# Optimization experiments

Measured on AMD Instinct MI355X. Metric: run time of the kernel, lower is better.

Reference implementation:

```python
import jax, jax.numpy as jnp
import numpy as np

B, S, HID = 1, 2048, 2304
H, KV, D = 8, 4, 256
FF = 9216
CAP = 50.0                      # attn_logit_softcapping
SCALE = 256.0 ** -0.5           # query_pre_attn_scalar ** -0.5
WIN = 1024                      # sliding_window_size
EPS = 1e-6
NEG = -2.3819763e38


def setup_inputs() -> dict:
    key = jax.random.key(0)
    ks = jax.random.split(key, 11)
    w = lambda k, shp: jax.random.normal(k, shp, jnp.float32) * 0.02
    ln = lambda k: jax.random.normal(k, (HID,), jnp.float32) * 0.1
    hidden_states = jax.random.normal(ks[0], (B, S, HID), jnp.float32)
    qkv_w = w(ks[1], (HID, (H + 2 * KV) * D))
    o_w = w(ks[2], (H * D, HID))
    gate_w = w(ks[3], (HID, FF))
    up_w = w(ks[4], (HID, FF))
    down_w = w(ks[5], (FF, HID))
    in_ln_w = ln(ks[6]); post_attn_ln_w = ln(ks[7])
    pre_ffw_ln_w = ln(ks[8]); post_ffw_ln_w = ln(ks[9])
    # precompute_freqs_cis (theta=10000) as cos/sin of shape [S, D//2]
    inv = 1.0 / (10000.0 ** (np.arange(0, D, 2)[: D // 2].astype(np.float64) / D))
    fr = np.outer(np.arange(S), inv)
    cos = jnp.asarray(np.cos(fr), jnp.float32)
    sin = jnp.asarray(np.sin(fr), jnp.float32)
    kv_write_indices = jnp.arange(S, dtype=jnp.int32)
    k_cache = jnp.zeros((B, S, KV, D), jnp.float32)
    v_cache = jnp.zeros((B, S, KV, D), jnp.float32)
    causal = jnp.tril(jnp.ones((S, S), bool))
    mask = jnp.where(causal, 0.0, NEG).astype(jnp.float32)[None, None]
    return dict(hidden_states=hidden_states, qkv_w=qkv_w, o_w=o_w,
                gate_w=gate_w, up_w=up_w, down_w=down_w,
                in_ln_w=in_ln_w, post_attn_ln_w=post_attn_ln_w,
                pre_ffw_ln_w=pre_ffw_ln_w, post_ffw_ln_w=post_ffw_ln_w,
                cos=cos, sin=sin, kv_write_indices=kv_write_indices,
                k_cache=k_cache, v_cache=v_cache, mask=mask)


def rmsnorm(x, wt):
    x = x.astype(jnp.float32)
    x = x * jax.lax.rsqrt(jnp.mean(x * x, axis=-1, keepdims=True) + EPS)
    return x * (1.0 + wt)  # add_unit_offset=True


def rope(x, cos, sin):
    # x: [b,s,h,d]; complex rotation with real=first half, imag=second half
    x1, x2 = jnp.split(x, 2, axis=-1)
    c = cos[None, :, None, :]
    s = sin[None, :, None, :]
    return jnp.concatenate([x1 * c - x2 * s, x1 * s + x2 * c], axis=-1)


def reference(hidden_states, qkv_w, o_w, gate_w, up_w, down_w,
              in_ln_w, post_attn_ln_w, pre_ffw_ln_w, post_ffw_ln_w,
              cos, sin, kv_write_indices, k_cache, v_cache, mask):
    residual = hidden_states
    x = rmsnorm(hidden_states, in_ln_w)
    qkv = x @ qkv_w
    q = qkv[..., : H * D].reshape(B, S, H, D)
    k = qkv[..., H * D: H * D + KV * D].reshape(B, S, KV, D)
    v = qkv[..., H * D + KV * D:].reshape(B, S, KV, D)
    q = rope(q, cos, sin)
    k = rope(k, cos, sin)
    kc = k_cache.at[:, kv_write_indices].set(k)
    vc = v_cache.at[:, kv_write_indices].set(v)
    g = H // KV
    kr = jnp.repeat(kc, g, axis=2)   # GQA repeat_interleave -> [B,S,H,D]
    vr = jnp.repeat(vc, g, axis=2)
    scores = jnp.einsum('bqhd,bkhd->bhqk', q * SCALE, kr)
    pos = jnp.arange(S)
    band = jnp.abs(pos[:, None] - pos[None, :]) <= (WIN - 1)
    m = jnp.where(band[None, None], mask, NEG)
    scores = jnp.tanh(scores / CAP) * CAP + m
    probs = jax.nn.softmax(scores.astype(jnp.float32), axis=-1)
    attn = jnp.einsum('bhqk,bkhd->bqhd', probs, vr).reshape(B, S, H * D)
    attn = attn @ o_w
    h = residual + rmsnorm(attn, post_attn_ln_w)
    residual = h
    x = rmsnorm(h, pre_ffw_ln_w)
    x = jax.nn.gelu(x @ gate_w, approximate=True) * (x @ up_w)
    x = x @ down_w
    x = rmsnorm(x, post_ffw_ln_w)
    return residual + x
```

## Files before the change

### kernel.cpp

```cpp
#include <hip/hip_runtime.h>
#include <hip/hip_bf16.h>
#include <cstdint>
#include <cstddef>

#define S_LEN  2048
#define HIDDEN 2304
#define NHEAD  8
#define NKVH   4
#define DHEAD  256
#define FFDIM  9216
#define QKVN   4096
#define ODIM   2048
#define WINM1  1023
#define QSCALE 0.0625f
#define CAPF   50.0f
#define PSTR   ((size_t)S_LEN * HIDDEN)

typedef __attribute__((ext_vector_type(4))) float f32x4;
typedef __attribute__((ext_vector_type(8))) short s16x8;

__device__ __forceinline__ void gload_lds16(const void* gptr, void* lptr) {
  __builtin_amdgcn_global_load_lds(
      (const __attribute__((address_space(1))) unsigned int*)gptr,
      (__attribute__((address_space(3))) unsigned int*)lptr, 16, 0, 0);
}

__global__ void k_fill(float* p, float v, size_t n) {
  size_t i = (size_t)blockIdx.x * blockDim.x + threadIdx.x;
  size_t st = (size_t)gridDim.x * blockDim.x;
  for (; i < n; i += st) p[i] = v;
}

__global__ void k_transpose_bf16(const float* __restrict__ in, __hip_bfloat16* __restrict__ out,
                                 int R, int C) {
  __shared__ float tile[32][33];
  const int c0 = blockIdx.x * 32, r0 = blockIdx.y * 32;
  const int tc = threadIdx.x & 31, tr = threadIdx.x >> 5;
#pragma unroll
  for (int i = 0; i < 4; i++)
    tile[tr + 8 * i][tc] = in[(size_t)(r0 + tr + 8 * i) * C + c0 + tc];
  __syncthreads();
#pragma unroll
  for (int i = 0; i < 4; i++)
    out[(size_t)(c0 + tr + 8 * i) * R + r0 + tc] = __float2bfloat16(tile[tc][tr + 8 * i]);
}

template <int NP, bool INBF16, bool ADD, bool BF16OUT>
__global__ void k_rmsnorm(const void* __restrict__ xv, const float* __restrict__ w,
                          const float* __restrict__ res, void* __restrict__ outv) {
  const int row = blockIdx.x;
  __shared__ float xs[HIDDEN];
  float ss = 0.f;
  for (int i = threadIdx.x; i < HIDDEN; i += 256) {
    float v = 0.f;
#pragma unroll
    for (int p = 0; p < NP; p++) {
      if constexpr (INBF16)
        v += __bfloat162float(((const __hip_bfloat16*)xv)[(size_t)p * PSTR + (size_t)row * HIDDEN + i]);
      else
        v += ((const float*)xv)[(size_t)p * PSTR + (size_t)row * HIDDEN + i];
    }
    xs[i] = v;
    ss += v * v;
  }
#pragma unroll
  for (int off = 32; off >= 1; off >>= 1) ss += __shfl_down(ss, off);
  __shared__ float red[4];
  __shared__ float srstd;
  if ((threadIdx.x & 63) == 0) red[threadIdx.x >> 6] = ss;
  __syncthreads();
  if (threadIdx.x == 0) {
    float tot = red[0] + red[1] + red[2] + red[3];
    srstd = rsqrtf(tot / (float)HIDDEN + 1e-6f);
  }
  __syncthreads();
  const float rstd = srstd;
  for (int i = threadIdx.x; i < HIDDEN; i += 256) {
    float v = xs[i] * rstd * (1.f + w[i]);
    if constexpr (ADD) v += res[(size_t)row * HIDDEN + i];
    if constexpr (BF16OUT)
      ((__hip_bfloat16*)outv)[(size_t)row * HIDDEN + i] = __float2bfloat16(v);
    else
      ((float*)outv)[(size_t)row * HIDDEN + i] = v;
  }
}

template <int EPI>
__global__ __launch_bounds__(256) void k_gemm_bt(const __hip_bfloat16* __restrict__ A,
                                                 const __hip_bfloat16* __restrict__ Bt,
                                                 void* __restrict__ Cv,
                                                 const __hip_bfloat16* __restrict__ G,
                                                 int N, int K) {
  __shared__ alignas(16) __hip_bfloat16 sA[128 * 64];
  __shared__ alignas(16) __hip_bfloat16 sB[128 * 64];
  const int t = threadIdx.x;
  const int w = t >> 6;
  const int wm = w >> 1, wn = w & 1;
  const int nwg = gridDim.x * gridDim.y;
  const int fblk = blockIdx.y * gridDim.x + blockIdx.x;
  const int qq = nwg >> 3, r8 = nwg & 7;
  const int xcd = fblk & 7, ix = fblk >> 3;
  const int swz = (xcd < r8 ? xcd * (qq + 1) : r8 * (qq + 1) + (xcd - r8) * qq) + ix;
  const int m0 = (swz % gridDim.y) * 128, n0 = (swz / gridDim.y) * 128;
  const int lr = t & 15, lg = (t & 63) >> 4;
  const int srow = t >> 3, sc8 = t & 7;

  f32x4 acc[4][4];
#pragma unroll
  for (int a = 0; a < 4; a++)
#pragma unroll
    for (int b = 0; b < 4; b++) acc[a][b] = (f32x4){0.f, 0.f, 0.f, 0.f};

  for (int kt = 0; kt < K; kt += 64) {
#pragma unroll
    for (int i = 0; i < 4; i++) {
      const __hip_bfloat16* g = A + (size_t)(m0 + i * 32 + srow) * K + kt + sc8 * 8;
      gload_lds16(g, sA + (size_t)(i * 256 + w * 64) * 8);
    }
#pragma unroll
    for (int i = 0; i < 4; i++) {
      const __hip_bfloat16* g = Bt + (size_t)(n0 + i * 32 + srow) * K + kt + sc8 * 8;
      gload_lds16(g, sB + (size_t)(i * 256 + w * 64) * 8);
    }
    __syncthreads();
#pragma unroll
    for (int ks = 0; ks < 2; ks++) {
      s16x8 af[4], bfr[4];
#pragma unroll
      for (int fm = 0; fm < 4; fm++)
        af[fm] = *reinterpret_cast<const s16x8*>(sA + (wm * 64 + fm * 16 + lr) * 64 + ks * 32 + lg * 8);
#pragma unroll
      for (int fn = 0; fn < 4; fn++)
        bfr[fn] = *reinterpret_cast<const s16x8*>(sB + (wn * 64 + fn * 16 + lr) * 64 + ks * 32 + lg * 8);
#pragma unroll
      for (int fm = 0; fm < 4; fm++)
#pragma unroll
        for (int fn = 0; fn < 4; fn++)
          acc[fm][fn] = __builtin_amdgcn_mfma_f32_16x16x32_bf16(af[fm], bfr[fn], acc[fm][fn], 0, 0, 0);
    }
    __syncthreads();
  }
#pragma unroll
  for (int fm = 0; fm < 4; fm++) {
    const int rb = m0 + wm * 64 + fm * 16 + lg * 4;
#pragma unroll
    for (int fn = 0; fn < 4; fn++) {
      const int col = n0 + wn * 64 + fn * 16 + lr;
#pragma unroll
      for (int j = 0; j < 4; j++) {
        const size_t idx = (size_t)(rb + j) * N + col;
        if constexpr (EPI == 0) {
          ((float*)Cv)[idx] = acc[fm][fn][j];
        } else if constexpr (EPI == 1) {
          ((__hip_bfloat16*)Cv)[idx] = __float2bfloat16(acc[fm][fn][j]);
        } else {
          const float x = __bfloat162float(G[idx]);
          const float tt = tanhf(0.7978845608028654f * (x + 0.044715f * x * x * x));
          ((__hip_bfloat16*)Cv)[idx] = __float2bfloat16(0.5f * x * (1.f + tt) * acc[fm][fn][j]);
        }
      }
    }
  }
}

template <int EPI>
__global__ __launch_bounds__(512, 2) void k_gemm8(const __hip_bfloat16* __restrict__ A,
                                                  const __hip_bfloat16* __restrict__ Bt,
                                                  void* __restrict__ Cv,
                                                  const __hip_bfloat16* __restrict__ G,
                                                  const __hip_bfloat16* __restrict__ Bt2,
                                                  void* __restrict__ Cv2,
                                                  int N, int K, int keff) {
  __shared__ alignas(16) __hip_bfloat16 smem[65536];
  const int t = threadIdx.x;
  const int w = t >> 6;
  const int wm = w >> 2, wn = w & 3;
  const int l = t & 63;
  const int lr = l & 15, lg = l >> 4;

  const int nxy = gridDim.x * gridDim.y;
  const int nwg = nxy * gridDim.z;
  const int fblk = blockIdx.z * nxy + blockIdx.y * gridDim.x + blockIdx.x;
  const int qq = nwg >> 3, r8 = nwg & 7;
  const int xcd = fblk & 7, ix = fblk >> 3;
  const int swz = (xcd < r8 ? xcd * (qq + 1) : r8 * (qq + 1) + (xcd - r8) * qq) + ix;
  const int plane = swz / nxy;
  const int rem = swz % nxy;
  const int m0 = (rem % gridDim.y) * 256, n0 = (rem / gridDim.y) * 256;
  const int k0 = plane * keff;

  const __hip_bfloat16* Bsrc = Bt;
  int nb0 = n0;
  if constexpr (EPI == 3) {
    if (n0 >= FFDIM) { Bsrc = Bt2; nb0 = n0 - FFDIM; }
  }

  const int sA8 = l & 7;
  size_t aoff[2], boff[2];
#pragma unroll
  for (int j = 0; j < 2; j++) {
    const int rv = (w * 2 + j) * 8 + (l >> 3);
    const int ko = (sA8 ^ (rv & 7)) * 8;
    aoff[j] = (size_t)(m0 + ((rv >> 6) & 1) * 128 + ((rv >> 4) & 3) * 16 + (rv & 15)) * K + k0 + ko;
    boff[j] = (size_t)(nb0 + ((rv >> 5) & 3) * 64 + ((rv >> 4) & 1) * 16 + (rv & 15)) * K + k0 + ko;
  }
  const int sl0 = ((lg) ^ (lr & 7)) * 8;
  const int sl1 = ((4 + lg) ^ (lr & 7)) * 8;

  f32x4 acc[8][4];
#pragma unroll
  for (int a = 0; a < 8; a++)
#pragma unroll
    for (int b = 0; b < 4; b++) acc[a][b] = (f32x4){0.f, 0.f, 0.f, 0.f};
  s16x8 af[4][2], bf[2][2];

#define STG_A(bu, h, kti) { _Pragma("unroll") for (int j = 0; j < 2; j++) \
    gload_lds16(A + aoff[j] + (size_t)(h) * 64 * K + (size_t)(kti) * 64, \
                smem + (bu) * 32768 + (h) * 8192 + (w * 2 + j) * 512); }
#define STG_B(bu, h, kti) { _Pragma("unroll") for (int j = 0; j < 2; j++) \
    gload_lds16(Bsrc + boff[j] + (size_t)(h) * 32 * K + (size_t)(kti) * 64, \
                smem + (bu) * 32768 + 16384 + (h) * 8192 + (w * 2 + j) * 512); }
#define RD_A(bu, fmh) { const __hip_bfloat16* ab_ = smem + (bu) * 32768; \
    _Pragma("unroll") for (int f2 = 0; f2 < 4; f2++) { \
      const int ro_ = ((fmh) * 128 + wm * 64 + f2 * 16 + lr) * 64; \
      af[f2][0] = *(const s16x8*)(ab_ + ro_ + sl0); \
      af[f2][1] = *(const s16x8*)(ab_ + ro_ + sl1); } }
#define RD_B(bu, fnh) { const __hip_bfloat16* bb_ = smem + (bu) * 32768 + 16384; \
    _Pragma("unroll") for (int f2 = 0; f2 < 2; f2++) { \
      const int ro_ = ((fnh) * 128 + wn * 32 + f2 * 16 + lr) * 64; \
      bf[f2][0] = *(const s16x8*)(bb_ + ro_ + sl0); \
      bf[f2][1] = *(const s16x8*)(bb_ + ro_ + sl1); } }
#define MFMA16(fmh, fnh) { __builtin_amdgcn_s_setprio(1); \
    _Pragma("unroll") for (int f2 = 0; f2 < 4; f2++) \
    _Pragma("unroll") for (int g2 = 0; g2 < 2; g2++) \
    _Pragma("unroll") for (int ks = 0; ks < 2; ks++) \
      acc[(fmh) * 4 + f2][(fnh) * 2 + g2] = __builtin_amdgcn_mfma_f32_16x16x32_bf16( \
          af[f2][ks], bf[g2][ks], acc[(fmh) * 4 + f2][(fnh) * 2 + g2], 0, 0, 0); \
    __builtin_amdgcn_s_setprio(0); }
#define BARR() asm volatile("s_barrier" ::: "memory")
#define LGKM0() asm volatile("s_waitcnt lgkmcnt(0)" ::: "memory")
#define VMC4() asm volatile("s_waitcnt vmcnt(4)" ::: "memory")
#define VMC0() asm volatile("s_waitcnt vmcnt(0)" ::: "memory")

  STG_A(0, 0, 0); STG_A(0, 1, 0); STG_B(0, 0, 0); STG_B(0, 1, 0);
  STG_A(1, 0, 1); STG_A(1, 1, 1);
  VMC4(); BARR();

  const int niter = keff >> 7;
  for (int i = 0; i < niter; ++i) {
    const int t1 = 2 * i + 1;
    const bool more = (i + 1 < niter);
    RD_A(0, 0); RD_B(0, 0);
    STG_B(1, 0, t1);
    BARR(); LGKM0(); MFMA16(0, 0); BARR();
    RD_B(0, 1);
    STG_B(1, 1, t1);
    if (more) STG_A(0, 0, t1 + 1);
    BARR(); LGKM0(); MFMA16(0, 1); BARR();
    RD_A(0, 1); RD_B(0, 0);
    BARR(); LGKM0(); MFMA16(1, 0); BARR();
    RD_B(0, 1);
    if (more) STG_A(0, 1, t1 + 1);
    BARR(); LGKM0(); MFMA16(1, 1);
    if (more) { VMC4(); } else { VMC0(); }
    BARR();
    RD_A(1, 0); RD_B(1, 0);
    if (more) STG_B(0, 0, t1 + 1);
    BARR(); LGKM0(); MFMA16(0, 0); BARR();
    RD_B(1, 1);
    if (more) STG_B(0, 1, t1 + 1);
    BARR(); LGKM0(); MFMA16(0, 1); BARR();
    RD_A(1, 1); RD_B(1, 0);
    if (more) STG_A(1, 0, t1 + 2);
    BARR(); LGKM0(); MFMA16(1, 0); BARR();
    RD_B(1, 1);
    if (more) STG_A(1, 1, t1 + 2);
    BARR(); LGKM0(); MFMA16(1, 1);
    if (more) { VMC4(); }
    BARR();
  }
#undef STG_A
#undef STG_B
#undef RD_A
#undef RD_B
#undef MFMA16
#undef BARR
#undef LGKM0
#undef VMC4
#undef VMC0

  __hip_bfloat16* Cw = nullptr;
  int cbase = n0, cstride = N;
  if constexpr (EPI == 3) {
    Cw = (__hip_bfloat16*)((n0 < FFDIM) ? Cv : Cv2);
    cbase = (n0 < FFDIM) ? n0 : n0 - FFDIM;
    cstride = FFDIM;
  }
#pragma unroll
  for (int fm = 0; fm < 8; fm++) {
    const int rb = m0 + wm * 128 + fm * 16 + lg * 4;
#pragma unroll
    for (int fn = 0; fn < 4; fn++) {
      const int coln = wn * 64 + fn * 16 + lr;
#pragma unroll
      for (int j = 0; j < 4; j++) {
        if constexpr (EPI == 3) {
          Cw[(size_t)(rb + j) * cstride + cbase + coln] = __float2bfloat16(acc[fm][fn][j]);
        } else {
          const size_t idxo = (size_t)(rb + j) * N + n0 + coln;
          if constexpr (EPI == 0) {
            ((float*)Cv)[idxo] = acc[fm][fn][j];
          } else if constexpr (EPI == 1) {
            ((__hip_bfloat16*)Cv)[idxo] = __float2bfloat16(acc[fm][fn][j]);
          } else if constexpr (EPI == 2) {
            const float x = __bfloat162float(G[idxo]);
            const float tg = tanhf(0.7978845608028654f * (x + 0.044715f * x * x * x));
            ((__hip_bfloat16*)Cv)[idxo] = __float2bfloat16(0.5f * x * (1.f + tg) * acc[fm][fn][j]);
          } else if constexpr (EPI == 4) {
            float* P = (plane == 0) ? (float*)Cv : (float*)Cv2;
            P[idxo] = acc[fm][fn][j];
          } else {
            ((__hip_bfloat16*)Cv)[(size_t)plane * PSTR + idxo] = __float2bfloat16(acc[fm][fn][j]);
          }
        }
      }
    }
  }
}

__global__ void k_gelu_mul2(const __hip_bfloat16* __restrict__ g, const __hip_bfloat16* __restrict__ u,
                            __hip_bfloat16* __restrict__ o, int n8) {
  const int st = gridDim.x * blockDim.x;
  for (int i = blockIdx.x * blockDim.x + threadIdx.x; i < n8; i += st) {
    s16x8 gv = *(const s16x8*)(g + (size_t)i * 8);
    s16x8 uv = *(const s16x8*)(u + (size_t)i * 8);
    s16x8 ov;
#pragma unroll
    for (int j = 0; j < 8; j++) {
      const float x = __uint_as_float(((uint32_t)(uint16_t)gv[j]) << 16);
      const float uu = __uint_as_float(((uint32_t)(uint16_t)uv[j]) << 16);
      const float tt = tanhf(0.7978845608028654f * (x + 0.044715f * x * x * x));
      const float r = 0.5f * x * (1.f + tt) * uu;
      ov[j] = (short)(__hip_bfloat16_raw(__float2bfloat16(r)).x);
    }
    *(s16x8*)(o + (size_t)i * 8) = ov;
  }
}

__global__ void k_rope_split(const float* __restrict__ p0, const float* __restrict__ p1,
                             const float* __restrict__ cosb, const float* __restrict__ sinb,
                             __hip_bfloat16* __restrict__ qo, __hip_bfloat16* __restrict__ ko) {
  const int s = blockIdx.x;
  const float* r0 = p0 + (size_t)s * QKVN;
  const float* r1 = p1 + (size_t)s * QKVN;
  const float* cr = cosb + (size_t)s * 128;
  const float* sr = sinb + (size_t)s * 128;
  for (int idx = threadIdx.x; idx < (NHEAD + NKVH) * 128; idx += 256) {
    const int hh = idx >> 7, d = idx & 127;
    const float cv = cr[d], sv = sr[d];
    if (hh < NHEAD) {
      const float x1 = r0[hh * DHEAD + d] + r1[hh * DHEAD + d];
      const float x2 = r0[hh * DHEAD + 128 + d] + r1[hh * DHEAD + 128 + d];
      const size_t base = ((size_t)hh * S_LEN + s) * DHEAD;
      qo[base + d]       = __float2bfloat16((x1 * cv - x2 * sv) * QSCALE);
      qo[base + 128 + d] = __float2bfloat16((x1 * sv + x2 * cv) * QSCALE);
    } else {
      const int kv = hh - NHEAD;
      const int o1 = NHEAD * DHEAD + kv * DHEAD + d;
      const float x1 = r0[o1] + r1[o1];
      const float x2 = r0[o1 + 128] + r1[o1 + 128];
      const size_t base = ((size_t)kv * S_LEN + s) * DHEAD;
      ko[base + d]       = __float2bfloat16(x1 * cv - x2 * sv);
      ko[base + 128 + d] = __float2bfloat16(x1 * sv + x2 * cv);
    }
  }
}

__global__ __launch_bounds__(256) void k_vsplit_t(const float* __restrict__ p0,
                                                  const float* __restrict__ p1,
                                                  __hip_bfloat16* __restrict__ vt) {
  __shared__ float tile[64][260];
  const int s0 = blockIdx.x * 64, kv = blockIdx.y;
  const int t = threadIdx.x;
  const int rr = t >> 6, c4 = t & 63;
#pragma unroll
  for (int p = 0; p < 16; p++) {
    const int row = rr + p * 4;
    const size_t go = (size_t)(s0 + row) * QKVN + (NHEAD + NKVH) * DHEAD + kv * DHEAD + c4 * 4;
    const float4 v0 = *(const float4*)(p0 + go);
    const float4 v1 = *(const float4*)(p1 + go);
    float4 v;
    v.x = v0.x + v1.x; v.y = v0.y + v1.y; v.z = v0.z + v1.z; v.w = v0.w + v1.w;
    *(float4*)(&tile[row][c4 * 4]) = v;
  }
  __syncthreads();
  const int c = t & 31, dr = t >> 5;
#pragma unroll
  for (int p = 0; p < 32; p++) {
    const int d = dr + p * 8;
    __hip_bfloat162 pr;
    pr.x = __float2bfloat16(tile[2 * c][d]);
    pr.y = __float2bfloat16(tile[2 * c + 1][d]);
    *(__hip_bfloat162*)(vt + ((size_t)kv * DHEAD + d) * S_LEN + s0 + 2 * c) = pr;
  }
}

__global__ __launch_bounds__(256) void k_attn_mfma(const __hip_bfloat16* __restrict__ Q,
                                                   const __hip_bfloat16* __restrict__ Kb,
                                                   const __hip_bfloat16* __restrict__ Vt,
                                                   __hip_bfloat16* __restrict__ O) {
  __shared__ alignas(16) __hip_bfloat16 Ks[64 * 264];
  __shared__ alignas(16) __hip_bfloat16 Vs[256 * 72];
  __shared__ alignas(16) __hip_bfloat16 Ps[64 * 72];
  const int h = blockIdx.y, kvh = h >> 1;
  const int q0 = blockIdx.x * 64;
  const int t = threadIdx.x;
  const int wq = t >> 6;
  const int l = t & 63;
  const int lr = l & 15, lg = l >> 4;

  s16x8 qf[8];
  {
    const __hip_bfloat16* qrow = Q + ((size_t)h * S_LEN + q0 + wq * 16 + lr) * DHEAD;
#pragma unroll
    for (int ks = 0; ks < 8; ks++) qf[ks] = *(const s16x8*)(qrow + ks * 32 + lg * 8);
  }
  f32x4 acc[16];
#pragma unroll
  for (int i = 0; i < 16; i++) acc[i] = (f32x4){0.f, 0.f, 0.f, 0.f};
  float rsum[4] = {0.f, 0.f, 0.f, 0.f};

  int lo = q0 - WINM1;
  if (lo < 0) lo = 0;
  lo &= ~63;
  const int qrow_base = q0 + wq * 16 + lg * 4;

  for (int kc = lo; kc <= q0; kc += 64) {
#pragma unroll
    for (int p = 0; p < 8; p++) {
      const int idx = t + p * 256;
      const int row = idx >> 5, c16 = idx & 31;
      s16x8 v = *(const s16x8*)(Kb + ((size_t)kvh * S_LEN + kc + row) * DHEAD + c16 * 8);
      *(s16x8*)(Ks + row * 264 + c16 * 8) = v;
    }
#pragma unroll
    for (int p = 0; p < 8; p++) {
      const int idx = t + p * 256;
      const int d = idx >> 3, ch = idx & 7;
      s16x8 v = *(const s16x8*)(Vt + ((size_t)kvh * DHEAD + d) * S_LEN + kc + ch * 8);
      *(s16x8*)(Vs + d * 72 + ch * 8) = v;
    }
    __syncthreads();

    f32x4 sc[4];
#pragma unroll
    for (int fq = 0; fq < 4; fq++) {
      sc[fq] = (f32x4){0.f, 0.f, 0.f, 0.f};
#pragma unroll
      for (int ks = 0; ks < 8; ks++) {
        s16x8 bfr = *(const s16x8*)(Ks + (fq * 16 + lr) * 264 + ks * 32 + lg * 8);
        sc[fq] = __builtin_amdgcn_mfma_f32_16x16x32_bf16(qf[ks], bfr, sc[fq], 0, 0, 0);
      }
    }
#pragma unroll
    for (int fq = 0; fq < 4; fq++) {
      const int k = kc + fq * 16 + lr;
#pragma unroll
      for (int j = 0; j < 4; j++) {
        const int qw = qrow_base + j;
        float p = 0.f;
        if (k <= qw && qw - k <= WINM1) {
          const float s = sc[fq][j];
          const float u = exp2f(s * 0.057707801635558534f);
          const float arg = 72.134752044448169f -
                            144.26950408889634f * __builtin_amdgcn_rcpf(u + 1.f);
          p = exp2f(arg);
        }
        const __hip_bfloat16 pb = __float2bfloat16(p);
        Ps[(wq * 16 + lg * 4 + j) * 72 + fq * 16 + lr] = pb;
        rsum[j] += __bfloat162float(pb);
      }
    }
#pragma unroll
    for (int ks2 = 0; ks2 < 2; ks2++) {
      s16x8 pa = *(const s16x8*)(Ps + (wq * 16 + lr) * 72 + ks2 * 32 + lg * 8);
#pragma unroll
      for (int f2 = 0; f2 < 16; f2++) {
        s16x8 vb = *(const s16x8*)(Vs + (f2 * 16 + lr) * 72 + ks2 * 32 + lg * 8);
        acc[f2] = __builtin_amdgcn_mfma_f32_16x16x32_bf16(pa, vb, acc[f2], 0, 0, 0);
      }
    }
    __syncthreads();
  }
#pragma unroll
  for (int j = 0; j < 4; j++) {
    float s = rsum[j];
#pragma unroll
    for (int off = 1; off < 16; off <<= 1) s += __shfl_xor(s, off, 64);
    rsum[j] = 1.f / s;
  }
#pragma unroll
  for (int f2 = 0; f2 < 16; f2++)
#pragma unroll
    for (int j = 0; j < 4; j++)
      O[(size_t)(qrow_base + j) * ODIM + h * DHEAD + f2 * 16 + lr] =
          __float2bfloat16(acc[f2][j] * rsum[j]);
}

extern "C" void kernel_launch(void* const* d_in, const int* in_sizes, int n_in,
                              void* d_out, int out_size, void* d_ws, size_t ws_size,
                              hipStream_t stream) {
  const float* hidden  = (const float*)d_in[0];
  const float* qkv_w   = (const float*)d_in[1];
  const float* o_w     = (const float*)d_in[2];
  const float* gate_w  = (const float*)d_in[3];
  const float* up_w    = (const float*)d_in[4];
  const float* down_w  = (const float*)d_in[5];
  const float* in_ln   = (const float*)d_in[6];
  const float* post_attn_ln = (const float*)d_in[7];
  const float* pre_ffw_ln   = (const float*)d_in[8];
  const float* post_ffw_ln  = (const float*)d_in[9];
  const float* cosb    = (const float*)d_in[10];
  const float* sinb    = (const float*)d_in[11];
  float* out = (float*)d_out;
  char* ws = (char*)d_ws;

  const size_t OFF_W   = 0;
  const size_t OFF_HF  = 42467328;
  const size_t OFF_X   = 61341696;
  const size_t OFF_S1  = 70778880;
  const size_t OFF_S2  = 108527616;
  const size_t NEED    = 146276352;
  const size_t OFF_W2  = 146276352;
  const size_t NEED_F  = 188743680;

  if (ws_size < NEED) {
    k_fill<<<1024, 256, 0, stream>>>(out, 100000.0f + (float)(ws_size >> 20), (size_t)out_size);
    return;
  }
  const bool FUSED = (ws_size >= NEED_F);

  __hip_bfloat16* W    = (__hip_bfloat16*)(ws + OFF_W);
  __hip_bfloat16* W2   = (__hip_bfloat16*)(ws + OFF_W2);
  float*          Hf   = (float*)(ws + OFF_HF);
  __hip_bfloat16* Xb   = (__hip_bfloat16*)(ws + OFF_X);
  __hip_bfloat16* GATEB= (__hip_bfloat16*)(ws + OFF_S1);
  __hip_bfloat16* UPB  = (__hip_bfloat16*)(ws + OFF_S2);
  __hip_bfloat16* Qb   = (__hip_bfloat16*)(ws + OFF_S2);
  __hip_bfloat16* Kb   = (__hip_bfloat16*)(ws + OFF_S2 + 8388608);
  __hip_bfloat16* Vtb  = (__hip_bfloat16*)(ws + OFF_S2 + 12582912);
  __hip_bfloat16* ATTN = (__hip_bfloat16*)(ws + OFF_S2 + 29360128);

  if (FUSED) {
    float* QKV0 = (float*)(ws + OFF_S1);
    float* QKV1 = (float*)(ws + OFF_W2);
    float* PROJ = (float*)(ws + OFF_S1);
    __hip_bfloat16* DPART = (__hip_bfloat16*)(ws + OFF_S2);

    k_transpose_bf16<<<dim3(QKVN / 32, HIDDEN / 32), 256, 0, stream>>>(qkv_w, W, HIDDEN, QKVN);
    k_rmsnorm<1, false, false, true><<<S_LEN, 256, 0, stream>>>(hidden, in_ln, nullptr, Xb);
    k_gemm8<4><<<dim3(QKVN / 256, S_LEN / 256, 2), 512, 0, stream>>>(
        Xb, W, QKV0, nullptr, nullptr, QKV1, QKVN, HIDDEN, HIDDEN / 2);
    k_rope_split<<<S_LEN, 256, 0, stream>>>(QKV0, QKV1, cosb, sinb, Qb, Kb);
    k_vsplit_t<<<dim3(S_LEN / 64, NKVH), 256, 0, stream>>>(QKV0, QKV1, Vtb);
    k_attn_mfma<<<dim3(S_LEN / 64, NHEAD), 256, 0, stream>>>(Qb, Kb, Vtb, ATTN);
    k_transpose_bf16<<<dim3(HIDDEN / 32, ODIM / 32), 256, 0, stream>>>(o_w, W, ODIM, HIDDEN);
    k_gemm8<4><<<dim3(HIDDEN / 256, S_LEN / 256, 2), 512, 0, stream>>>(
        ATTN, W, PROJ, nullptr, nullptr, PROJ + PSTR, HIDDEN, ODIM, ODIM / 2);
    k_rmsnorm<2, false, true, false><<<S_LEN, 256, 0, stream>>>(PROJ, post_attn_ln, hidden, Hf);
    k_rmsnorm<1, false, false, true><<<S_LEN, 256, 0, stream>>>(Hf, pre_ffw_ln, nullptr, Xb);
    k_transpose_bf16<<<dim3(FFDIM / 32, HIDDEN / 32), 256, 0, stream>>>(gate_w, W, HIDDEN, FFDIM);
    k_transpose_bf16<<<dim3(FFDIM / 32, HIDDEN / 32), 256, 0, stream>>>(up_w, W2, HIDDEN, FFDIM);
    k_gemm8<3><<<dim3((2 * FFDIM) / 256, S_LEN / 256, 1), 512, 0, stream>>>(
        Xb, W, GATEB, nullptr, W2, UPB, FFDIM, HIDDEN, HIDDEN);
    k_gelu_mul2<<<2048, 256, 0, stream>>>(GATEB, UPB, GATEB, (S_LEN * FFDIM) / 8);
    k_transpose_bf16<<<dim3(HIDDEN / 32, FFDIM / 32), 256, 0, stream>>>(down_w, W, FFDIM, HIDDEN);
    k_gemm8<5><<<dim3(HIDDEN / 256, S_LEN / 256, 8), 512, 0, stream>>>(
        GATEB, W, DPART, nullptr, nullptr, nullptr, HIDDEN, FFDIM, FFDIM / 8);
    k_rmsnorm<8, true, true, false><<<S_LEN, 256, 0, stream>>>(DPART, post_ffw_ln, Hf, out);
  } else {
    float* QKV = (float*)(ws + OFF_S1);
    float* PROJ = (float*)(ws + OFF_S2);
    k_transpose_bf16<<<dim3(QKVN / 32, HIDDEN / 32), 256, 0, stream>>>(qkv_w, W, HIDDEN, QKVN);
    k_rmsnorm<1, false, false, true><<<S_LEN, 256, 0, stream>>>(hidden, in_ln, nullptr, Xb);
    k_gemm_bt<0><<<dim3(QKVN / 128, S_LEN / 128), 256, 0, stream>>>(Xb, W, QKV, nullptr, QKVN, HIDDEN);
    k_rope_split<<<S_LEN, 256, 0, stream>>>(QKV, QKV, cosb, sinb, Qb, Kb);
    k_fill<<<1024, 256, 0, stream>>>(Hf, 0.f, PSTR);
    k_rope_split<<<S_LEN, 256, 0, stream>>>(QKV, Hf, cosb, sinb, Qb, Kb);
    k_vsplit_t<<<dim3(S_LEN / 64, NKVH), 256, 0, stream>>>(QKV, Hf, Vtb);
    k_attn_mfma<<<dim3(S_LEN / 64, NHEAD), 256, 0, stream>>>(Qb, Kb, Vtb, ATTN);
    k_transpose_bf16<<<dim3(HIDDEN / 32, ODIM / 32), 256, 0, stream>>>(o_w, W, ODIM, HIDDEN);
    k_gemm_bt<0><<<dim3(HIDDEN / 128, S_LEN / 128), 256, 0, stream>>>(ATTN, W, PROJ, nullptr, HIDDEN, ODIM);
    k_rmsnorm<1, false, true, false><<<S_LEN, 256, 0, stream>>>(PROJ, post_attn_ln, hidden, Hf);
    k_rmsnorm<1, false, false, true><<<S_LEN, 256, 0, stream>>>(Hf, pre_ffw_ln, nullptr, Xb);
    k_transpose_bf16<<<dim3(FFDIM / 32, HIDDEN / 32), 256, 0, stream>>>(gate_w, W, HIDDEN, FFDIM);
    k_gemm8<1><<<dim3(FFDIM / 256, S_LEN / 256, 1), 512, 0, stream>>>(
        Xb, W, GATEB, nullptr, nullptr, nullptr, FFDIM, HIDDEN, HIDDEN);
    __hip_bfloat16* ACT = (__hip_bfloat16*)(ws + OFF_S2);
    k_transpose_bf16<<<dim3(FFDIM / 32, HIDDEN / 32), 256, 0, stream>>>(up_w, W, HIDDEN, FFDIM);
    k_gemm8<2><<<dim3(FFDIM / 256, S_LEN / 256, 1), 512, 0, stream>>>(
        Xb, W, ACT, GATEB, nullptr, nullptr, FFDIM, HIDDEN, HIDDEN);
    float* Yf = (float*)(ws + OFF_S1);
    k_transpose_bf16<<<dim3(HIDDEN / 32, FFDIM / 32), 256, 0, stream>>>(down_w, W, FFDIM, HIDDEN);
    k_gemm_bt<0><<<dim3(HIDDEN / 128, S_LEN / 128), 256, 0, stream>>>(ACT, W, Yf, nullptr, HIDDEN, FFDIM);
    k_rmsnorm<1, false, true, false><<<S_LEN, 256, 0, stream>>>(Yf, post_ffw_ln, Hf, out);
  }
}
```

Before: 700.2 us.

## Add half-height 128x256 GEMM kernel for FFN and fuse double rmsnorm

Adds k_gemm8h, a 128x256-tile variant of the 8-wave GEMM with a smaller LDS footprint and launch_bounds(512,2), so two workgroups can share a CU. It is used for the fused gate/up GEMM and the split-K down projection, which also doubles the number of tiles. The post-attention rmsnorm and pre-FFN rmsnorm are merged into one kernel to cut a launch and a round trip of the hidden state. The fallback path is trimmed and moved onto k_gemm_bt. The tradeoff is less data reuse per tile and extra A-tile loads.

```diff
diff --git a/kernel.cpp b/kernel.cpp
--- a/kernel.cpp
+++ b/kernel.cpp
@@ -83,6 +83,48 @@
     else
       ((float*)outv)[(size_t)row * HIDDEN + i] = v;
   }
+}
+
+__global__ void k_rmsnorm2(const float* __restrict__ planes, const float* __restrict__ w1,
+                           const float* __restrict__ res, const float* __restrict__ w2,
+                           float* __restrict__ hf, __hip_bfloat16* __restrict__ xb) {
+  const int row = blockIdx.x;
+  __shared__ float xs[HIDDEN];
+  __shared__ float red[4];
+  __shared__ float srstd;
+  float ss = 0.f;
+  for (int i = threadIdx.x; i < HIDDEN; i += 256) {
+    const float v = planes[(size_t)row * HIDDEN + i] + planes[PSTR + (size_t)row * HIDDEN + i];
+    xs[i] = v;
+    ss += v * v;
+  }
+#pragma unroll
+  for (int off = 32; off >= 1; off >>= 1) ss += __shfl_down(ss, off);
+  if ((threadIdx.x & 63) == 0) red[threadIdx.x >> 6] = ss;
+  __syncthreads();
+  if (threadIdx.x == 0)
+    srstd = rsqrtf((red[0] + red[1] + red[2] + red[3]) / (float)HIDDEN + 1e-6f);
+  __syncthreads();
+  const float rstd1 = srstd;
+  float ss2 = 0.f;
+  for (int i = threadIdx.x; i < HIDDEN; i += 256) {
+    const float h = res[(size_t)row * HIDDEN + i] + xs[i] * rstd1 * (1.f + w1[i]);
+    hf[(size_t)row * HIDDEN + i] = h;
+    ss2 += h * h;
+  }
+  __syncthreads();
+  for (int i = threadIdx.x; i < HIDDEN; i += 256)
+    xs[i] = hf[(size_t)row * HIDDEN + i];
+#pragma unroll
+  for (int off = 32; off >= 1; off >>= 1) ss2 += __shfl_down(ss2, off);
+  if ((threadIdx.x & 63) == 0) red[threadIdx.x >> 6] = ss2;
+  __syncthreads();
+  if (threadIdx.x == 0)
+    srstd = rsqrtf((red[0] + red[1] + red[2] + red[3]) / (float)HIDDEN + 1e-6f);
+  __syncthreads();
+  const float rstd2 = srstd;
+  for (int i = threadIdx.x; i < HIDDEN; i += 256)
+    xb[(size_t)row * HIDDEN + i] = __float2bfloat16(xs[i] * rstd2 * (1.f + w2[i]));
 }
 
 template <int EPI>
@@ -189,12 +231,6 @@
   const int m0 = (rem % gridDim.y) * 256, n0 = (rem / gridDim.y) * 256;
   const int k0 = plane * keff;
 
-  const __hip_bfloat16* Bsrc = Bt;
-  int nb0 = n0;
-  if constexpr (EPI == 3) {
-    if (n0 >= FFDIM) { Bsrc = Bt2; nb0 = n0 - FFDIM; }
-  }
-
   const int sA8 = l & 7;
   size_t aoff[2], boff[2];
 #pragma unroll
@@ -202,7 +238,7 @@
     const int rv = (w * 2 + j) * 8 + (l >> 3);
     const int ko = (sA8 ^ (rv & 7)) * 8;
     aoff[j] = (size_t)(m0 + ((rv >> 6) & 1) * 128 + ((rv >> 4) & 3) * 16 + (rv & 15)) * K + k0 + ko;
-    boff[j] = (size_t)(nb0 + ((rv >> 5) & 3) * 64 + ((rv >> 4) & 1) * 16 + (rv & 15)) * K + k0 + ko;
+    boff[j] = (size_t)(n0 + ((rv >> 5) & 3) * 64 + ((rv >> 4) & 1) * 16 + (rv & 15)) * K + k0 + ko;
   }
   const int sl0 = ((lg) ^ (lr & 7)) * 8;
   const int sl1 = ((4 + lg) ^ (lr & 7)) * 8;
@@ -218,7 +254,7 @@
     gload_lds16(A + aoff[j] + (size_t)(h) * 64 * K + (size_t)(kti) * 64, \
                 smem + (bu) * 32768 + (h) * 8192 + (w * 2 + j) * 512); }
 #define STG_B(bu, h, kti) { _Pragma("unroll") for (int j = 0; j < 2; j++) \
-    gload_lds16(Bsrc + boff[j] + (size_t)(h) * 32 * K + (size_t)(kti) * 64, \
+    gload_lds16(Bt + boff[j] + (size_t)(h) * 32 * K + (size_t)(kti) * 64, \
                 smem + (bu) * 32768 + 16384 + (h) * 8192 + (w * 2 + j) * 512); }
 #define RD_A(bu, fmh) { const __hip_bfloat16* ab_ = smem + (bu) * 32768; \
     _Pragma("unroll") for (int f2 = 0; f2 < 4; f2++) { \
@@ -289,41 +325,158 @@
 #undef VMC4
 #undef VMC0
 
-  __hip_bfloat16* Cw = nullptr;
-  int cbase = n0, cstride = N;
+#pragma unroll
+  for (int fm = 0; fm < 8; fm++) {
+    const int rb = m0 + wm * 128 + fm * 16 + lg * 4;
+#pragma unroll
+    for (int fn = 0; fn < 4; fn++) {
+      const int coln = wn * 64 + fn * 16 + lr;
+#pragma unroll
+      for (int j = 0; j < 4; j++) {
+        const size_t idxo = (size_t)(rb + j) * N + n0 + coln;
+        if constexpr (EPI == 4) {
+          float* P = (plane == 0) ? (float*)Cv : (float*)Cv2;
+          P[idxo] = acc[fm][fn][j];
+        } else {
+          ((__hip_bfloat16*)Cv)[idxo] = __float2bfloat16(acc[fm][fn][j]);
+        }
+      }
+    }
+  }
+}
+
+template <int EPI>
+__global__ __launch_bounds__(512, 2) void k_gemm8h(const __hip_bfloat16* __restrict__ A,
+                                                   const __hip_bfloat16* __restrict__ Bt,
+                                                   void* __restrict__ Cv,
+                                                   const __hip_bfloat16* __restrict__ Bt2,
+                                                   void* __restrict__ Cv2,
+                                                   int N, int K, int keff) {
+  __shared__ alignas(16) __hip_bfloat16 smem[49152];
+  const int t = threadIdx.x;
+  const int w = t >> 6;
+  const int wm = w >> 2, wn = w & 3;
+  const int l = t & 63;
+  const int lr = l & 15, lg = l >> 4;
+
+  const int nxy = gridDim.x * gridDim.y;
+  const int nwg = nxy * gridDim.z;
+  const int fblk = blockIdx.z * nxy + blockIdx.y * gridDim.x + blockIdx.x;
+  const int qq = nwg >> 3, r8 = nwg & 7;
+  const int xcd = fblk & 7, ix = fblk >> 3;
+  const int swz = (xcd < r8 ? xcd * (qq + 1) : r8 * (qq + 1) + (xcd - r8) * qq) + ix;
+  const int plane = swz / nxy;
+  const int rem = swz % nxy;
+  const int m0 = (rem % gridDim.y) * 128, n0 = (rem / gridDim.y) * 256;
+  const int k0 = plane * keff;
+
+  const __hip_bfloat16* Bsrc = Bt;
+  int nb0 = n0;
+  if constexpr (EPI == 3) {
+    if (n0 >= FFDIM) { Bsrc = Bt2; nb0 = n0 - FFDIM; }
+  }
+
+  const int lrow = w * 8 + (l >> 3);
+  const int ko = (((l & 7) ^ (l >> 3))) * 8;
+  const size_t aoffh = (size_t)(m0 + lrow) * K + k0 + ko;
+  const size_t boffh = (size_t)(nb0 + lrow) * K + k0 + ko;
+  const int sl0 = ((lg) ^ (lr & 7)) * 8;
+  const int sl1 = ((4 + lg) ^ (lr & 7)) * 8;
+
+  f32x4 acc[4][4];
+#pragma unroll
+  for (int a = 0; a < 4; a++)
+#pragma unroll
+    for (int b = 0; b < 4; b++) acc[a][b] = (f32x4){0.f, 0.f, 0.f, 0.f};
+  s16x8 af[4][2], bf[2][2];
+
+#define HSTG_A(bu, kti) { _Pragma("unroll") for (int j = 0; j < 2; j++) \
+    gload_lds16(A + aoffh + (size_t)j * 64 * K + (size_t)(kti) * 64, \
+                smem + (bu) * 24576 + (j * 64 + w * 8) * 64); }
+#define HSTG_B0(bu, kti) { _Pragma("unroll") for (int j = 0; j < 2; j++) \
+    gload_lds16(Bsrc + boffh + (size_t)j * 64 * K + (size_t)(kti) * 64, \
+                smem + (bu) * 24576 + 8192 + (j * 64 + w * 8) * 64); }
+#define HSTG_B1(bu, kti) { _Pragma("unroll") for (int j = 2; j < 4; j++) \
+    gload_lds16(Bsrc + boffh + (size_t)j * 64 * K + (size_t)(kti) * 64, \
+                smem + (bu) * 24576 + 8192 + (j * 64 + w * 8) * 64); }
+#define HRD_A(bu) { const __hip_bfloat16* ab_ = smem + (bu) * 24576; \
+    _Pragma("unroll") for (int f2 = 0; f2 < 4; f2++) { \
+      const int ro_ = (wm * 64 + f2 * 16 + lr) * 64; \
+      af[f2][0] = *(const s16x8*)(ab_ + ro_ + sl0); \
+      af[f2][1] = *(const s16x8*)(ab_ + ro_ + sl1); } }
+#define HRD_B(bu, fnh) { const __hip_bfloat16* bb_ = smem + (bu) * 24576 + 8192; \
+    _Pragma("unroll") for (int f2 = 0; f2 < 2; f2++) { \
+      const int ro_ = ((fnh) * 128 + wn * 32 + f2 * 16 + lr) * 64; \
+      bf[f2][0] = *(const s16x8*)(bb_ + ro_ + sl0); \
+      bf[f2][1] = *(const s16x8*)(bb_ + ro_ + sl1); } }
+#define HMFMA16(fnh) { __builtin_amdgcn_s_setprio(1); \
+    _Pragma("unroll") for (int f2 = 0; f2 < 4; f2++) \
+    _Pragma("unroll") for (int g2 = 0; g2 < 2; g2++) \
+    _Pragma("unroll") for (int ks = 0; ks < 2; ks++) \
+      acc[f2][(fnh) * 2 + g2] = __builtin_amdgcn_mfma_f32_16x16x32_bf16( \
+          af[f2][ks], bf[g2][ks], acc[f2][(fnh) * 2 + g2], 0, 0, 0); \
+    __builtin_amdgcn_s_setprio(0); }
+#define HBARR() asm volatile("s_barrier" ::: "memory")
+#define HLGKM0() asm volatile("s_waitcnt lgkmcnt(0)" ::: "memory")
+#define HVMC4() asm volatile("s_waitcnt vmcnt(4)" ::: "memory")
+#define HVMC0() asm volatile("s_waitcnt vmcnt(0)" ::: "memory")
+
+  HSTG_A(0, 0); HSTG_B0(0, 0); HSTG_B1(0, 0);
+  HSTG_A(1, 1); HSTG_B0(1, 1);
+  HVMC4(); HBARR();
+
+  const int niter = keff >> 7;
+  for (int i = 0; i < niter; ++i) {
+    const int t1 = 2 * i + 1;
+    const bool more = (i + 1 < niter);
+    HRD_A(0); HRD_B(0, 0);
+    HSTG_B1(1, t1);
+    HBARR(); HLGKM0(); HMFMA16(0); HBARR();
+    HRD_B(0, 1);
+    if (more) { HSTG_A(0, t1 + 1); HSTG_B0(0, t1 + 1); }
+    HBARR(); HLGKM0(); HMFMA16(1);
+    if (more) { HVMC4(); } else { HVMC0(); }
+    HBARR();
+    HRD_A(1); HRD_B(1, 0);
+    if (more) HSTG_B1(0, t1 + 1);
+    HBARR(); HLGKM0(); HMFMA16(0); HBARR();
+    HRD_B(1, 1);
+    if (more) { HSTG_A(1, t1 + 2); HSTG_B0(1, t1 + 2); }
+    HBARR(); HLGKM0(); HMFMA16(1);
+    if (more) { HVMC4(); }
+    HBARR();
+  }
+#undef HSTG_A
+#undef HSTG_B0
+#undef HSTG_B1
+#undef HRD_A
+#undef HRD_B
+#undef HMFMA16
+#undef HBARR
+#undef HLGKM0
+#undef HVMC4
+#undef HVMC0
+
+  __hip_bfloat16* Cw;
+  int cbase, cstride;
   if constexpr (EPI == 3) {
     Cw = (__hip_bfloat16*)((n0 < FFDIM) ? Cv : Cv2);
     cbase = (n0 < FFDIM) ? n0 : n0 - FFDIM;
     cstride = FFDIM;
-  }
-#pragma unroll
-  for (int fm = 0; fm < 8; fm++) {
-    const int rb = m0 + wm * 128 + fm * 16 + lg * 4;
+  } else {
+    Cw = (__hip_bfloat16*)Cv + (size_t)plane * PSTR;
+    cbase = n0;
+    cstride = N;
+  }
+#pragma unroll
+  for (int fm = 0; fm < 4; fm++) {
+    const int rb = m0 + wm * 64 + fm * 16 + lg * 4;
 #pragma unroll
     for (int fn = 0; fn < 4; fn++) {
-      const int coln = wn * 64 + fn * 16 + lr;
-#pragma unroll
-      for (int j = 0; j < 4; j++) {
-        if constexpr (EPI == 3) {
-          Cw[(size_t)(rb + j) * cstride + cbase + coln] = __float2bfloat16(acc[fm][fn][j]);
-        } else {
-          const size_t idxo = (size_t)(rb + j) * N + n0 + coln;
-          if constexpr (EPI == 0) {
-            ((float*)Cv)[idxo] = acc[fm][fn][j];
-          } else if constexpr (EPI == 1) {
-            ((__hip_bfloat16*)Cv)[idxo] = __float2bfloat16(acc[fm][fn][j]);
-          } else if constexpr (EPI == 2) {
-            const float x = __bfloat162float(G[idxo]);
-            const float tg = tanhf(0.7978845608028654f * (x + 0.044715f * x * x * x));
-            ((__hip_bfloat16*)Cv)[idxo] = __float2bfloat16(0.5f * x * (1.f + tg) * acc[fm][fn][j]);
-          } else if constexpr (EPI == 4) {
-            float* P = (plane == 0) ? (float*)Cv : (float*)Cv2;
-            P[idxo] = acc[fm][fn][j];
-          } else {
-            ((__hip_bfloat16*)Cv)[(size_t)plane * PSTR + idxo] = __float2bfloat16(acc[fm][fn][j]);
-          }
-        }
-      }
+      const int coln = (fn >> 1) * 128 + wn * 32 + (fn & 1) * 16 + lr;
+#pragma unroll
+      for (int j = 0; j < 4; j++)
+        Cw[(size_t)(rb + j) * cstride + cbase + coln] = __float2bfloat16(acc[fm][fn][j]);
     }
   }
 }
@@ -567,16 +720,15 @@
     k_transpose_bf16<<<dim3(HIDDEN / 32, ODIM / 32), 256, 0, stream>>>(o_w, W, ODIM, HIDDEN);
     k_gemm8<4><<<dim3(HIDDEN / 256, S_LEN / 256, 2), 512, 0, stream>>>(
         ATTN, W, PROJ, nullptr, nullptr, PROJ + PSTR, HIDDEN, ODIM, ODIM / 2);
-    k_rmsnorm<2, false, true, false><<<S_LEN, 256, 0, stream>>>(PROJ, post_attn_ln, hidden, Hf);
-    k_rmsnorm<1, false, false, true><<<S_LEN, 256, 0, stream>>>(Hf, pre_ffw_ln, nullptr, Xb);
+    k_rmsnorm2<<<S_LEN, 256, 0, stream>>>(PROJ, post_attn_ln, hidden, pre_ffw_ln, Hf, Xb);
     k_transpose_bf16<<<dim3(FFDIM / 32, HIDDEN / 32), 256, 0, stream>>>(gate_w, W, HIDDEN, FFDIM);
     k_transpose_bf16<<<dim3(FFDIM / 32, HIDDEN / 32), 256, 0, stream>>>(up_w, W2, HIDDEN, FFDIM);
-    k_gemm8<3><<<dim3((2 * FFDIM) / 256, S_LEN / 256, 1), 512, 0, stream>>>(
-        Xb, W, GATEB, nullptr, W2, UPB, FFDIM, HIDDEN, HIDDEN);
+    k_gemm8h<3><<<dim3((2 * FFDIM) / 256, S_LEN / 128, 1), 512, 0, stream>>>(
+        Xb, W, GATEB, W2, UPB, FFDIM, HIDDEN, HIDDEN);
     k_gelu_mul2<<<2048, 256, 0, stream>>>(GATEB, UPB, GATEB, (S_LEN * FFDIM) / 8);
     k_transpose_bf16<<<dim3(HIDDEN / 32, FFDIM / 32), 256, 0, stream>>>(down_w, W, FFDIM, HIDDEN);
-    k_gemm8<5><<<dim3(HIDDEN / 256, S_LEN / 256, 8), 512, 0, stream>>>(
-        GATEB, W, DPART, nullptr, nullptr, nullptr, HIDDEN, FFDIM, FFDIM / 8);
+    k_gemm8h<5><<<dim3(HIDDEN / 256, S_LEN / 128, 8), 512, 0, stream>>>(
+        GATEB, W, DPART, nullptr, nullptr, HIDDEN, FFDIM, FFDIM / 8);
     k_rmsnorm<8, true, true, false><<<S_LEN, 256, 0, stream>>>(DPART, post_ffw_ln, Hf, out);
   } else {
     float* QKV = (float*)(ws + OFF_S1);
@@ -584,7 +736,6 @@
     k_transpose_bf16<<<dim3(QKVN / 32, HIDDEN / 32), 256, 0, stream>>>(qkv_w, W, HIDDEN, QKVN);
     k_rmsnorm<1, false, false, true><<<S_LEN, 256, 0, stream>>>(hidden, in_ln, nullptr, Xb);
     k_gemm_bt<0><<<dim3(QKVN / 128, S_LEN / 128), 256, 0, stream>>>(Xb, W, QKV, nullptr, QKVN, HIDDEN);
-    k_rope_split<<<S_LEN, 256, 0, stream>>>(QKV, QKV, cosb, sinb, Qb, Kb);
     k_fill<<<1024, 256, 0, stream>>>(Hf, 0.f, PSTR);
     k_rope_split<<<S_LEN, 256, 0, stream>>>(QKV, Hf, cosb, sinb, Qb, Kb);
     k_vsplit_t<<<dim3(S_LEN / 64, NKVH), 256, 0, stream>>>(QKV, Hf, Vtb);
@@ -594,12 +745,10 @@
     k_rmsnorm<1, false, true, false><<<S_LEN, 256, 0, stream>>>(PROJ, post_attn_ln, hidden, Hf);
     k_rmsnorm<1, false, false, true><<<S_LEN, 256, 0, stream>>>(Hf, pre_ffw_ln, nullptr, Xb);
     k_transpose_bf16<<<dim3(FFDIM / 32, HIDDEN / 32), 256, 0, stream>>>(gate_w, W, HIDDEN, FFDIM);
-    k_gemm8<1><<<dim3(FFDIM / 256, S_LEN / 256, 1), 512, 0, stream>>>(
-        Xb, W, GATEB, nullptr, nullptr, nullptr, FFDIM, HIDDEN, HIDDEN);
+    k_gemm_bt<1><<<dim3(FFDIM / 128, S_LEN / 128), 256, 0, stream>>>(Xb, W, GATEB, nullptr, FFDIM, HIDDEN);
     __hip_bfloat16* ACT = (__hip_bfloat16*)(ws + OFF_S2);
     k_transpose_bf16<<<dim3(FFDIM / 32, HIDDEN / 32), 256, 0, stream>>>(up_w, W, HIDDEN, FFDIM);
-    k_gemm8<2><<<dim3(FFDIM / 256, S_LEN / 256, 1), 512, 0, stream>>>(
-        Xb, W, ACT, GATEB, nullptr, nullptr, FFDIM, HIDDEN, HIDDEN);
+    k_gemm_bt<2><<<dim3(FFDIM / 128, S_LEN / 128), 256, 0, stream>>>(Xb, W, ACT, GATEB, FFDIM, HIDDEN);
     float* Yf = (float*)(ws + OFF_S1);
     k_transpose_bf16<<<dim3(HIDDEN / 32, FFDIM / 32), 256, 0, stream>>>(down_w, W, FFDIM, HIDDEN);
     k_gemm_bt<0><<<dim3(HIDDEN / 128, S_LEN / 128), 256, 0, stream>>>(ACT, W, Yf, nullptr, HIDDEN, FFDIM);
```

After: 705.1 us. Within noise of the previous version (+0.7%).
